# Kernel optimization log

Hardware: AMD Instinct MI355X
Metric: run time of the kernel (lower is better)

## Reference

```python
import jax, jax.numpy as jnp
import numpy as np

B, N, DIM = 8, 4096, 512
H, DH = 8, 64
INNER = H * DH
MIN_FREQ = 1.0 / 64
SCALE = 1.0
ROT_DIM = DH // 2  # 32, per spatial axis
EPS = 1e-5


def setup_inputs() -> dict:
    key = jax.random.key(0)
    ks = jax.random.split(key, 6)
    x = jax.random.normal(ks[0], (B, N, DIM), dtype=jnp.float32)
    pos = jax.random.uniform(ks[1], (B, N, 2), dtype=jnp.float32)
    W_qkv = jax.random.normal(ks[2], (3 * INNER, DIM), dtype=jnp.float32) * (1.0 / DH)
    gamma_k = jnp.ones((DH,), jnp.float32)
    beta_k = jnp.zeros((DH,), jnp.float32)
    gamma_v = jnp.ones((DH,), jnp.float32)
    beta_v = jnp.zeros((DH,), jnp.float32)
    W_out = jax.random.normal(ks[3], (DIM, INNER), dtype=jnp.float32) * (1.0 / np.sqrt(INNER))
    b_out = jnp.zeros((DIM,), jnp.float32)
    return {"x": x, "pos": pos, "W_qkv": W_qkv, "gamma_k": gamma_k, "beta_k": beta_k,
            "gamma_v": gamma_v, "beta_v": beta_v, "W_out": W_out, "b_out": b_out}


def _layernorm(t, gamma, beta):
    mu = jnp.mean(t, axis=-1, keepdims=True)
    var = jnp.var(t, axis=-1, keepdims=True)
    return (t - mu) * jax.lax.rsqrt(var + EPS) * gamma + beta


def _rotate_half(t):
    # '... (j d) -> ... j d' with j=2, then cat(-x2, x1)
    d = t.shape[-1] // 2
    x1, x2 = t[..., :d], t[..., d:]
    return jnp.concatenate((-x2, x1), axis=-1)


def _apply_rot(t, freqs):
    return t * jnp.cos(freqs) + _rotate_half(t) * jnp.sin(freqs)


def _freqs(coord):
    # coord: [b, n]; inv_freq over rotary half-dim
    inv_freq = 1.0 / (10000.0 ** (jnp.arange(0, ROT_DIM, 2, dtype=jnp.float32) / ROT_DIM))
    t = coord * (SCALE / MIN_FREQ)
    f = t[..., None] * inv_freq  # [b, n, ROT_DIM//2]
    return jnp.concatenate((f, f), axis=-1)[:, None, :, :]  # [b, 1, n, ROT_DIM]


def reference(x, pos, W_qkv, gamma_k, beta_k, gamma_v, beta_v, W_out, b_out):
    b, n, _ = x.shape
    qkv = x @ W_qkv.T  # [b, n, 3*INNER]
    q, k, v = jnp.split(qkv, 3, axis=-1)
    split = lambda t: t.reshape(b, n, H, DH).transpose(0, 2, 1, 3)  # b h n d
    q, k, v = split(q), split(k), split(v)

    # Galerkin: LayerNorm on K and V over head dim
    k = _layernorm(k, gamma_k, beta_k)
    v = _layernorm(v, gamma_v, beta_v)

    # 2D rotary on q, k: first half of head dim uses x-coords, second half y-coords
    fx, fy = _freqs(pos[..., 0]), _freqs(pos[..., 1])
    rot2d = lambda t: jnp.concatenate(
        (_apply_rot(t[..., :ROT_DIM], fx), _apply_rot(t[..., ROT_DIM:], fy)), axis=-1)
    q = rot2d(q)
    k = rot2d(k)

    # Associative linear attention: (K^T V) then Q @ (.) / n
    dots = jnp.einsum('bhnd,bhne->bhde', k, v)  # [b, h, d, d]
    out = jnp.einsum('bhnd,bhde->bhne', q, dots) * (1.0 / n)
    out = out.transpose(0, 2, 1, 3).reshape(b, n, INNER)
    return out @ W_out.T + b_out
```

## Files before the change

### kernel.cpp

```cpp
#include <hip/hip_runtime.h>
#include <math.h>

#define NB 8
#define NN 4096
#define NDIM 512
#define NH 8
#define NDH 64
#define QKVC 1536
#define NROWS (NB * NN)
#define EPSF 1e-5f
#define INV_N (1.0f / 4096.0f)
#define L2_10K_16 0.8304820237218406f

typedef __bf16 bf16x8_t __attribute__((ext_vector_type(8)));
typedef float f32x4_t __attribute__((ext_vector_type(4)));
typedef unsigned short u16x8 __attribute__((ext_vector_type(8)));

__device__ inline unsigned short f2bf(float f) {
    unsigned u = __builtin_bit_cast(unsigned, f);
    u += 0x7fff + ((u >> 16) & 1);
    return (unsigned short)(u >> 16);
}
__device__ inline float bf2f(unsigned short u) {
    unsigned v = (unsigned)u << 16;
    return __builtin_bit_cast(float, v);
}

#define GLOAD_LDS16(g, s) __builtin_amdgcn_global_load_lds(                    \
    (const __attribute__((address_space(1))) void*)(g),                        \
    (__attribute__((address_space(3))) void*)(s), 16, 0, 0)

__global__ __launch_bounds__(256)
void cvt_bf16_kernel(const float* __restrict__ s, unsigned short* __restrict__ d, int n)
{
    const int i = (blockIdx.x * 256 + threadIdx.x) * 8;
    if (i >= n) return;
    float4 a = *(const float4*)(s + i);
    float4 b = *(const float4*)(s + i + 4);
    ushort4 lo, hi;
    lo.x = f2bf(a.x); lo.y = f2bf(a.y); lo.z = f2bf(a.z); lo.w = f2bf(a.w);
    hi.x = f2bf(b.x); hi.y = f2bf(b.y); hi.z = f2bf(b.z); hi.w = f2bf(b.w);
    *(ushort4*)(d + i)     = lo;
    *(ushort4*)(d + i + 4) = hi;
}

__global__ __launch_bounds__(256)
void cvt_dots_kernel(const float* __restrict__ s, unsigned short* __restrict__ d)
{
    const int i = (blockIdx.x * 256 + threadIdx.x) * 4;
    float4 a = *(const float4*)(s + i);
    ushort4 o;
    o.x = f2bf(a.x * INV_N); o.y = f2bf(a.y * INV_N);
    o.z = f2bf(a.z * INV_N); o.w = f2bf(a.w * INV_N);
    *(ushort4*)(d + i) = o;
}

__global__ __launch_bounds__(512, 2)
void gemm_qkv_fused(const unsigned short* __restrict__ A,
                    const unsigned short* __restrict__ Bm,
                    const float* __restrict__ pos,
                    const float* __restrict__ gk, const float* __restrict__ bk,
                    const float* __restrict__ gv, const float* __restrict__ bvv,
                    unsigned short* __restrict__ qb,
                    unsigned short* __restrict__ kT,
                    unsigned short* __restrict__ vT)
{
    __shared__ __align__(16) unsigned short lds[2 * 32768];

    const int tid  = threadIdx.x;
    const int wave = tid >> 6;
    const int lane = tid & 63;

    int flat = blockIdx.y * 6 + blockIdx.x;
    flat = (flat & 7) * 96 + (flat >> 3);
    const int bx = flat % 6;
    const int by = flat / 6;
    const int m0 = by * 256;
    const int n0 = bx * 256;

    const int warp_m = wave >> 2;
    const int warp_n = wave & 3;
    const int fr = lane & 15;
    const int fq = lane >> 4;
    const int ch0 = ((fq ^ (fr & 7)) << 3);
    const int ch1 = ch0 ^ 32;

    const int r6 = tid >> 3;
    const int cs = (((tid & 7) ^ (r6 & 7)) << 3);
    const unsigned short* Asrc = A  + (size_t)(m0 + r6) * NDIM + cs;
    const unsigned short* Bsrc = Bm + (size_t)(n0 + (r6 >> 5) * 64 + (r6 & 31)) * NDIM + cs;
    const int sdst = wave * 512;

#define STG_A(tt, h, c) GLOAD_LDS16(Asrc + (size_t)((c) * 128 + (h) * 64) * NDIM + (tt) * 64, \
        &lds[(((tt) & 1) << 15) + ((h) << 13) + ((c) << 12) + sdst])
#define STG_B(tt, h, c) GLOAD_LDS16(Bsrc + (size_t)((c) * 128 + (h) * 32) * NDIM + (tt) * 64, \
        &lds[(((tt) & 1) << 15) + 16384 + ((h) << 13) + ((c) << 12) + sdst])
#define VMCNT4 asm volatile("s_waitcnt vmcnt(4)" ::: "memory")
#define BARF   { __builtin_amdgcn_s_barrier(); asm volatile("" ::: "memory"); }

    f32x4_t acc[8][4] = {};

    STG_A(0, 0, 0); STG_A(0, 0, 1);
    STG_B(0, 0, 0); STG_B(0, 0, 1);
    STG_B(0, 1, 0); STG_B(0, 1, 1);
    STG_A(0, 1, 0); STG_A(0, 1, 1);

    const unsigned short* Afr = &lds[(warp_m * 64 + fr) * 64];
    const unsigned short* Bfr = &lds[16384 + (warp_n * 32 + fr) * 64];

    bf16x8_t a0[4][2], a1[4][2], b0[2][2], b1[2][2];

    for (int tt = 0; tt < 7; ++tt) {
        const int rb = (tt & 1) << 15;
        VMCNT4; BARF;
        #pragma unroll
        for (int mi = 0; mi < 4; ++mi) {
            a0[mi][0] = *(const bf16x8_t*)&Afr[rb + mi * 1024 + ch0];
            a0[mi][1] = *(const bf16x8_t*)&Afr[rb + mi * 1024 + ch1];
        }
        #pragma unroll
        for (int nj = 0; nj < 2; ++nj) {
            b0[nj][0] = *(const bf16x8_t*)&Bfr[rb + nj * 1024 + ch0];
            b0[nj][1] = *(const bf16x8_t*)&Bfr[rb + nj * 1024 + ch1];
        }
        STG_A(tt + 1, 0, 0); STG_A(tt + 1, 0, 1);
        __builtin_amdgcn_s_setprio(1);
        #pragma unroll
        for (int mi = 0; mi < 4; ++mi)
            #pragma unroll
            for (int nj = 0; nj < 2; ++nj) {
                acc[mi][nj] = __builtin_amdgcn_mfma_f32_16x16x32_bf16(a0[mi][0], b0[nj][0], acc[mi][nj], 0, 0, 0);
                acc[mi][nj] = __builtin_amdgcn_mfma_f32_16x16x32_bf16(a0[mi][1], b0[nj][1], acc[mi][nj], 0, 0, 0);
            }
        __builtin_amdgcn_s_setprio(0);
        VMCNT4; BARF;
        #pragma unroll
        for (int nj = 0; nj < 2; ++nj) {
            b1[nj][0] = *(const bf16x8_t*)&Bfr[rb + 8192 + nj * 1024 + ch0];
            b1[nj][1] = *(const bf16x8_t*)&Bfr[rb + 8192 + nj * 1024 + ch1];
        }
        STG_B(tt + 1, 0, 0); STG_B(tt + 1, 0, 1);
        __builtin_amdgcn_s_setprio(1);
        #pragma unroll
        for (int mi = 0; mi < 4; ++mi)
            #pragma unroll
            for (int nj = 0; nj < 2; ++nj) {
                acc[mi][2 + nj] = __builtin_amdgcn_mfma_f32_16x16x32_bf16(a0[mi][0], b1[nj][0], acc[mi][2 + nj], 0, 0, 0);
                acc[mi][2 + nj] = __builtin_amdgcn_mfma_f32_16x16x32_bf16(a0[mi][1], b1[nj][1], acc[mi][2 + nj], 0, 0, 0);
            }
        __builtin_amdgcn_s_setprio(0);
        VMCNT4; BARF;
        #pragma unroll
        for (int mi = 0; mi < 4; ++mi) {
            a1[mi][0] = *(const bf16x8_t*)&Afr[rb + 8192 + mi * 1024 + ch0];
            a1[mi][1] = *(const bf16x8_t*)&Afr[rb + 8192 + mi * 1024 + ch1];
        }
        STG_B(tt + 1, 1, 0); STG_B(tt + 1, 1, 1);
        __builtin_amdgcn_s_setprio(1);
        #pragma unroll
        for (int mi = 0; mi < 4; ++mi)
            #pragma unroll
            for (int nj = 0; nj < 2; ++nj) {
                acc[4 + mi][nj] = __builtin_amdgcn_mfma_f32_16x16x32_bf16(a1[mi][0], b0[nj][0], acc[4 + mi][nj], 0, 0, 0);
                acc[4 + mi][nj] = __builtin_amdgcn_mfma_f32_16x16x32_bf16(a1[mi][1], b0[nj][1], acc[4 + mi][nj], 0, 0, 0);
            }
        __builtin_amdgcn_s_setprio(0);
        STG_A(tt + 1, 1, 0); STG_A(tt + 1, 1, 1);
        __builtin_amdgcn_s_setprio(1);
        #pragma unroll
        for (int mi = 0; mi < 4; ++mi)
            #pragma unroll
            for (int nj = 0; nj < 2; ++nj) {
                acc[4 + mi][2 + nj] = __builtin_amdgcn_mfma_f32_16x16x32_bf16(a1[mi][0], b1[nj][0], acc[4 + mi][2 + nj], 0, 0, 0);
                acc[4 + mi][2 + nj] = __builtin_amdgcn_mfma_f32_16x16x32_bf16(a1[mi][1], b1[nj][1], acc[4 + mi][2 + nj], 0, 0, 0);
            }
        __builtin_amdgcn_s_setprio(0);
    }
    {
        const int rb = 32768;
        asm volatile("s_waitcnt vmcnt(0)" ::: "memory");
        BARF;
        #pragma unroll
        for (int mi = 0; mi < 4; ++mi) {
            a0[mi][0] = *(const bf16x8_t*)&Afr[rb + mi * 1024 + ch0];
            a0[mi][1] = *(const bf16x8_t*)&Afr[rb + mi * 1024 + ch1];
        }
        #pragma unroll
        for (int nj = 0; nj < 2; ++nj) {
            b0[nj][0] = *(const bf16x8_t*)&Bfr[rb + nj * 1024 + ch0];
            b0[nj][1] = *(const bf16x8_t*)&Bfr[rb + nj * 1024 + ch1];
        }
        #pragma unroll
        for (int mi = 0; mi < 4; ++mi)
            #pragma unroll
            for (int nj = 0; nj < 2; ++nj) {
                acc[mi][nj] = __builtin_amdgcn_mfma_f32_16x16x32_bf16(a0[mi][0], b0[nj][0], acc[mi][nj], 0, 0, 0);
                acc[mi][nj] = __builtin_amdgcn_mfma_f32_16x16x32_bf16(a0[mi][1], b0[nj][1], acc[mi][nj], 0, 0, 0);
            }
        #pragma unroll
        for (int nj = 0; nj < 2; ++nj) {
            b1[nj][0] = *(const bf16x8_t*)&Bfr[rb + 8192 + nj * 1024 + ch0];
            b1[nj][1] = *(const bf16x8_t*)&Bfr[rb + 8192 + nj * 1024 + ch1];
        }
        #pragma unroll
        for (int mi = 0; mi < 4; ++mi)
            #pragma unroll
            for (int nj = 0; nj < 2; ++nj) {
                acc[mi][2 + nj] = __builtin_amdgcn_mfma_f32_16x16x32_bf16(a0[mi][0], b1[nj][0], acc[mi][2 + nj], 0, 0, 0);
                acc[mi][2 + nj] = __builtin_amdgcn_mfma_f32_16x16x32_bf16(a0[mi][1], b1[nj][1], acc[mi][2 + nj], 0, 0, 0);
            }
        #pragma unroll
        for (int mi = 0; mi < 4; ++mi) {
            a1[mi][0] = *(const bf16x8_t*)&Afr[rb + 8192 + mi * 1024 + ch0];
            a1[mi][1] = *(const bf16x8_t*)&Afr[rb + 8192 + mi * 1024 + ch1];
        }
        #pragma unroll
        for (int mi = 0; mi < 4; ++mi)
            #pragma unroll
            for (int nj = 0; nj < 2; ++nj) {
                acc[4 + mi][nj] = __builtin_amdgcn_mfma_f32_16x16x32_bf16(a1[mi][0], b0[nj][0], acc[4 + mi][nj], 0, 0, 0);
                acc[4 + mi][nj] = __builtin_amdgcn_mfma_f32_16x16x32_bf16(a1[mi][1], b0[nj][1], acc[4 + mi][nj], 0, 0, 0);
                acc[4 + mi][2 + nj] = __builtin_amdgcn_mfma_f32_16x16x32_bf16(a1[mi][0], b1[nj][0], acc[4 + mi][2 + nj], 0, 0, 0);
                acc[4 + mi][2 + nj] = __builtin_amdgcn_mfma_f32_16x16x32_bf16(a1[mi][1], b1[nj][1], acc[4 + mi][2 + nj], 0, 0, 0);
            }
    }
#undef STG_A
#undef STG_B
#undef VMCNT4
#undef BARF

    const int nc = n0 + warp_n * 64;
    const int type = nc >> 9;
    const int c  = lane & 15;
    const int g4 = (lane >> 4) * 4;
    const int mrow0 = m0 + warp_m * 128;

    if (type != 0) {
        const float* gamma = (type == 1) ? gk : gv;
        const float* beta  = (type == 1) ? bk : bvv;
        float gm[4], bt[4];
        #pragma unroll
        for (int j = 0; j < 4; ++j) { gm[j] = gamma[j * 16 + c]; bt[j] = beta[j * 16 + c]; }
        #pragma unroll
        for (int i = 0; i < 8; ++i)
            #pragma unroll
            for (int r = 0; r < 4; ++r) {
                float t0 = acc[i][0][r], t1 = acc[i][1][r];
                float t2 = acc[i][2][r], t3 = acc[i][3][r];
                float s  = t0 + t1 + t2 + t3;
                float ss = t0*t0 + t1*t1 + t2*t2 + t3*t3;
                #pragma unroll
                for (int msk = 1; msk < 16; msk <<= 1) {
                    s  += __shfl_xor(s,  msk, 64);
                    ss += __shfl_xor(ss, msk, 64);
                }
                const float mu = s * (1.0f / 64.0f);
                const float rs = rsqrtf(ss * (1.0f / 64.0f) - mu * mu + EPSF);
                acc[i][0][r] = (t0 - mu) * rs * gm[0] + bt[0];
                acc[i][1][r] = (t1 - mu) * rs * gm[1] + bt[1];
                acc[i][2][r] = (t2 - mu) * rs * gm[2] + bt[2];
                acc[i][3][r] = (t3 - mu) * rs * gm[3] + bt[3];
            }
    }
    if (type != 2) {
        const float Kc = 64.0f * exp2f(-(float)c * L2_10K_16);
        #pragma unroll
        for (int i = 0; i < 8; ++i)
            #pragma unroll
            for (int r = 0; r < 4; ++r) {
                const int row = mrow0 + (i >> 2) * 64 + (i & 3) * 16 + g4 + r;
                const float2 p = ((const float2*)pos)[row];
                float sx, cx, sy, cy;
                __sincosf(p.x * Kc, &sx, &cx);
                __sincosf(p.y * Kc, &sy, &cy);
                const float t0 = acc[i][0][r], t1 = acc[i][1][r];
                const float t2 = acc[i][2][r], t3 = acc[i][3][r];
                acc[i][0][r] = t0 * cx - t1 * sx;
                acc[i][1][r] = t1 * cx + t0 * sx;
                acc[i][2][r] = t2 * cy - t3 * sy;
                acc[i][3][r] = t3 * cy + t2 * sy;
            }
    }
    if (type == 0) {
        #pragma unroll
        for (int i = 0; i < 8; ++i)
            #pragma unroll
            for (int j = 0; j < 4; ++j) {
                unsigned short* qp = qb
                    + (size_t)(mrow0 + (i >> 2) * 64 + (i & 3) * 16 + g4) * NDIM
                    + nc + j * 16 + c;
                #pragma unroll
                for (int r = 0; r < 4; ++r)
                    qp[(size_t)r * NDIM] = f2bf(acc[i][j][r]);
            }
    } else {
        unsigned short* T = (type == 1) ? kT : vT;
        const int h = (nc >> 6) & 7;
        #pragma unroll
        for (int i = 0; i < 8; ++i) {
            const int row = mrow0 + (i >> 2) * 64 + (i & 3) * 16 + g4;
            const int bb = row >> 12;
            const int nl = row & 4095;
            #pragma unroll
            for (int j = 0; j < 4; ++j) {
                ushort4 o;
                o.x = f2bf(acc[i][j][0]); o.y = f2bf(acc[i][j][1]);
                o.z = f2bf(acc[i][j][2]); o.w = f2bf(acc[i][j][3]);
                *(ushort4*)(T + ((size_t)((bb * NH + h) * 64 + j * 16 + c)) * NN + nl) = o;
            }
        }
    }
}

__global__ __launch_bounds__(256)
void dots_mfma(const unsigned short* __restrict__ kT,
               const unsigned short* __restrict__ vT,
               float* __restrict__ dots)
{
    __shared__ __align__(16) unsigned short sk[2][64 * 64];
    __shared__ __align__(16) unsigned short sv[2][64 * 64];
    const int t = threadIdx.x;
    const int w = t >> 6, l = t & 63;
    const int bh = blockIdx.z * NH + blockIdx.y;
    const int n0 = blockIdx.x * 512;

    const int r8 = l >> 3;
    const int cs = ((l & 7) ^ r8) * 8;
    const unsigned short* ksrc = kT + (size_t)(bh * 64 + w * 16 + r8) * NN + n0 + cs;
    const unsigned short* vsrc = vT + (size_t)(bh * 64 + w * 16 + r8) * NN + n0 + cs;

#define STGK(buf, kt, q) GLOAD_LDS16(ksrc + (size_t)(q) * 8 * NN + (kt), \
        &sk[buf][w * 1024 + (q) * 512])
#define STGV(buf, kt, q) GLOAD_LDS16(vsrc + (size_t)(q) * 8 * NN + (kt), \
        &sv[buf][w * 1024 + (q) * 512])

    const int fr = l & 15, fq = l >> 4;
    const int doff = (w >> 1) * 32, eoff = (w & 1) * 32;

    f32x4_t acc[2][2] = {};

    STGK(0, 0, 0); STGK(0, 0, 1); STGV(0, 0, 0); STGV(0, 0, 1);

    for (int s = 0; s < 8; ++s) {
        const int buf = s & 1;
        asm volatile("s_waitcnt vmcnt(0)" ::: "memory");
        __builtin_amdgcn_s_barrier();
        bf16x8_t ak[2][2], bv[2][2];
        #pragma unroll
        for (int di = 0; di < 2; ++di)
            #pragma unroll
            for (int ks = 0; ks < 2; ++ks)
                ak[di][ks] = *(const bf16x8_t*)
                    &sk[buf][(doff + di * 16 + fr) * 64 + (((ks * 4 + fq) ^ (fr & 7)) * 8)];
        #pragma unroll
        for (int ej = 0; ej < 2; ++ej)
            #pragma unroll
            for (int ks = 0; ks < 2; ++ks)
                bv[ej][ks] = *(const bf16x8_t*)
                    &sv[buf][(eoff + ej * 16 + fr) * 64 + (((ks * 4 + fq) ^ (fr & 7)) * 8)];
        if (s + 1 < 8) {
            const int nb = buf ^ 1, kt = (s + 1) * 64;
            STGK(nb, kt, 0); STGK(nb, kt, 1); STGV(nb, kt, 0); STGV(nb, kt, 1);
        }
        #pragma unroll
        for (int ks = 0; ks < 2; ++ks)
            #pragma unroll
            for (int di = 0; di < 2; ++di)
                #pragma unroll
                for (int ej = 0; ej < 2; ++ej)
                    acc[di][ej] = __builtin_amdgcn_mfma_f32_16x16x32_bf16(
                        ak[di][ks], bv[ej][ks], acc[di][ej], 0, 0, 0);
    }
#undef STGK
#undef STGV

    float* dp = dots + (size_t)bh * 64 * 64;
    const int cc = l & 15;
    const int rr = (l >> 4) * 4;
    #pragma unroll
    for (int di = 0; di < 2; ++di)
        #pragma unroll
        for (int ej = 0; ej < 2; ++ej)
            #pragma unroll
            for (int r = 0; r < 4; ++r)
                atomicAdd(dp + (doff + di * 16 + rr + r) * 64 + eoff + ej * 16 + cc,
                          acc[di][ej][r]);
}

__global__ __launch_bounds__(256)
void dotsw_mfma(const unsigned short* __restrict__ Woutb,
                const unsigned short* __restrict__ dots_bf,
                unsigned short* __restrict__ M2b)
{
    __shared__ unsigned short As[128 * 64];
    __shared__ unsigned short Bs[64 * 64];
    const int t = threadIdx.x;
    const int wave = t >> 6;
    const int lane = t & 63;
    const int dp0 = blockIdx.x * 128;
    const int h = blockIdx.y, b = blockIdx.z;

    const int srow = lane >> 3;
    const int scol = (lane & 7) * 8;
    const unsigned short* Ag = Woutb + (size_t)(dp0 + wave * 32 + srow) * NDIM
                             + h * NDH + scol;
    const unsigned short* Bg = dots_bf + ((size_t)(b * NH + h) * 64 + wave * 16 + srow) * 64
                             + scol;
    #pragma unroll
    for (int i = 0; i < 4; ++i)
        GLOAD_LDS16(Ag + (size_t)i * 8 * NDIM, As + wave * 2048 + i * 512);
    #pragma unroll
    for (int i = 0; i < 2; ++i)
        GLOAD_LDS16(Bg + (size_t)i * 8 * 64, Bs + wave * 1024 + i * 512);
    __syncthreads();

    const int wm = (wave >> 1) * 64;
    const int wn = (wave & 1) * 32;
    const int fr = lane & 15;
    const int fq = (lane >> 4) * 8;

    f32x4_t acc[4][2] = {};
    #pragma unroll
    for (int kk = 0; kk < 2; ++kk) {
        bf16x8_t af[4], bf[2];
        #pragma unroll
        for (int i = 0; i < 4; ++i)
            af[i] = *(const bf16x8_t*)&As[(wm + i * 16 + fr) * 64 + kk * 32 + fq];
        #pragma unroll
        for (int j = 0; j < 2; ++j)
            bf[j] = *(const bf16x8_t*)&Bs[(wn + j * 16 + fr) * 64 + kk * 32 + fq];
        #pragma unroll
        for (int i = 0; i < 4; ++i)
            #pragma unroll
            for (int j = 0; j < 2; ++j)
                acc[i][j] = __builtin_amdgcn_mfma_f32_16x16x32_bf16(
                    af[i], bf[j], acc[i][j], 0, 0, 0);
    }

    const int c  = lane & 15;
    const int g4 = (lane >> 4) * 4;
    #pragma unroll
    for (int i = 0; i < 4; ++i)
        #pragma unroll
        for (int j = 0; j < 2; ++j) {
            unsigned short* mp = M2b + ((size_t)(b * NDIM) + dp0 + wm + i * 16 + g4) * NDIM
                               + h * NDH + wn + j * 16 + c;
            #pragma unroll
            for (int r = 0; r < 4; ++r)
                mp[(size_t)r * NDIM] = f2bf(acc[i][j][r]);
        }
}

__global__ __launch_bounds__(256)
void gemm_out_mfma(const unsigned short* __restrict__ qb,
                   const unsigned short* __restrict__ M2b,
                   const float* __restrict__ bias, float* __restrict__ C)
{
    __shared__ unsigned short As[128 * 32];
    __shared__ unsigned short Bs[128 * 32];
    const int t    = threadIdx.x;
    const int wave = t >> 6;
    const int lane = t & 63;
    const int b  = blockIdx.z;
    const int m0 = b * NN + blockIdx.y * 128;
    const int n0 = blockIdx.x * 128;
    const int wm = (wave >> 1) * 64;
    const int wn = (wave & 1) * 64;
    const int K = NDIM;

    f32x4_t acc[4][4] = {};

    const int srow = wave * 32 + (lane >> 2);
    const int scol = (lane & 3) * 8;
    const unsigned short* Ag = qb + (size_t)(m0 + srow) * NDIM + scol;
    const unsigned short* Bg = M2b + ((size_t)b * NDIM + n0 + srow) * NDIM + scol;
    unsigned short* sA = As + wave * 1024;
    unsigned short* sB = Bs + wave * 1024;

    const int fr = lane & 15;
    const int fq = (lane >> 4) * 8;

    for (int kt = 0; kt < K; kt += 32) {
        __syncthreads();
        GLOAD_LDS16(Ag + kt,             sA);
        GLOAD_LDS16(Ag + kt + 16 * NDIM, sA + 512);
        GLOAD_LDS16(Bg + kt,             sB);
        GLOAD_LDS16(Bg + kt + 16 * NDIM, sB + 512);
        __syncthreads();

        bf16x8_t af[4], bf[4];
        #pragma unroll
        for (int i = 0; i < 4; ++i) {
            af[i] = *(const bf16x8_t*)&As[(wm + i * 16 + fr) * 32 + fq];
            bf[i] = *(const bf16x8_t*)&Bs[(wn + i * 16 + fr) * 32 + fq];
        }
        #pragma unroll
        for (int i = 0; i < 4; ++i)
            #pragma unroll
            for (int j = 0; j < 4; ++j)
                acc[i][j] = __builtin_amdgcn_mfma_f32_16x16x32_bf16(
                    af[i], bf[j], acc[i][j], 0, 0, 0);
    }

    const int crow = (lane >> 4) * 4;
    const int ccol = lane & 15;
    #pragma unroll
    for (int j = 0; j < 4; ++j) {
        const int cn = n0 + wn + j * 16 + ccol;
        const float bb = bias[cn];
        #pragma unroll
        for (int i = 0; i < 4; ++i) {
            float* cp = C + (size_t)(m0 + wm + i * 16 + crow) * NDIM + cn;
            #pragma unroll
            for (int r = 0; r < 4; ++r)
                cp[(size_t)r * NDIM] = acc[i][j][r] + bb;
        }
    }
}

extern "C" void kernel_launch(void* const* d_in, const int* in_sizes, int n_in,
                              void* d_out, int out_size, void* d_ws, size_t ws_size,
                              hipStream_t stream)
{
    const float* x    = (const float*)d_in[0];
    const float* pos  = (const float*)d_in[1];
    const float* Wqkv = (const float*)d_in[2];
    const float* gk   = (const float*)d_in[3];
    const float* bk   = (const float*)d_in[4];
    const float* gv   = (const float*)d_in[5];
    const float* bv   = (const float*)d_in[6];
    const float* Wout = (const float*)d_in[7];
    const float* bout = (const float*)d_in[8];
    float* out = (float*)d_out;

    float* dots = (float*)d_ws;
    unsigned short* dots_bf = (unsigned short*)(dots + (size_t)NB * NH * 64 * 64);
    unsigned short* M2b     = dots_bf + (size_t)NB * NH * 64 * 64;
    unsigned short* qb      = M2b + (size_t)NB * NDIM * NDIM;
    unsigned short* kT      = qb + (size_t)NROWS * NDIM;
    unsigned short* vT      = kT + (size_t)NB * NH * NDH * NN;
    unsigned short* xb      = vT + (size_t)NB * NH * NDH * NN;
    unsigned short* Wqkvb   = xb + (size_t)NROWS * NDIM;
    unsigned short* Woutb   = Wqkvb + (size_t)QKVC * NDIM;

    hipMemsetAsync(dots, 0, (size_t)NB * NH * 64 * 64 * sizeof(float), stream);

    dim3 blk(256);
    cvt_bf16_kernel<<<dim3(NROWS * NDIM / 2048), blk, 0, stream>>>(x, xb, NROWS * NDIM);
    cvt_bf16_kernel<<<dim3(QKVC * NDIM / 2048), blk, 0, stream>>>(Wqkv, Wqkvb, QKVC * NDIM);
    cvt_bf16_kernel<<<dim3(NDIM * NDIM / 2048), blk, 0, stream>>>(Wout, Woutb, NDIM * NDIM);
    gemm_qkv_fused<<<dim3(QKVC / 256, NROWS / 256), dim3(512), 0, stream>>>(
        xb, Wqkvb, pos, gk, bk, gv, bv, qb, kT, vT);
    dots_mfma<<<dim3(NN / 512, NH, NB), blk, 0, stream>>>(kT, vT, dots);
    cvt_dots_kernel<<<dim3(NB * NH * 64 * 64 / 1024), blk, 0, stream>>>(dots, dots_bf);
    dotsw_mfma<<<dim3(NDIM / 128, NH, NB), blk, 0, stream>>>(Woutb, dots_bf, M2b);
    gemm_out_mfma<<<dim3(NDIM / 128, NN / 128, NB), blk, 0, stream>>>(
        qb, M2b, bout, out);
}
```

Before: 285.7 us.

## Fuse conversion kernels, fold dots cast into dotsw, pipeline 256x256 output GEMM

Three separate bf16 conversion launches and the memset of the dots buffer are merged into one cvt_all kernel. The dots-to-bf16 conversion and the 1/n scaling move into dotsw_mfma's shared-memory staging, which removes one launch and one intermediate buffer. The output GEMM is replaced with a 512-thread, 256x256-tile, double-buffered kernel that uses swizzled LDS, async global-to-LDS loads, setprio and grid remapping for cache locality. This cuts launch overhead and raises MFMA utilisation, at the cost of more registers per thread and more complex synchronisation.

```diff
diff --git a/kernel.cpp b/kernel.cpp
--- a/kernel.cpp
+++ b/kernel.cpp
@@ -30,11 +30,9 @@
     (const __attribute__((address_space(1))) void*)(g),                        \
     (__attribute__((address_space(3))) void*)(s), 16, 0, 0)
 
-__global__ __launch_bounds__(256)
-void cvt_bf16_kernel(const float* __restrict__ s, unsigned short* __restrict__ d, int n)
+__device__ inline void cvt8v(const float* __restrict__ s,
+                             unsigned short* __restrict__ d, int i)
 {
-    const int i = (blockIdx.x * 256 + threadIdx.x) * 8;
-    if (i >= n) return;
     float4 a = *(const float4*)(s + i);
     float4 b = *(const float4*)(s + i + 4);
     ushort4 lo, hi;
@@ -45,14 +43,23 @@
 }
 
 __global__ __launch_bounds__(256)
-void cvt_dots_kernel(const float* __restrict__ s, unsigned short* __restrict__ d)
+void cvt_all(const float* __restrict__ x,  const float* __restrict__ wq,
+             const float* __restrict__ wo,
+             unsigned short* __restrict__ xb, unsigned short* __restrict__ wqb,
+             unsigned short* __restrict__ wob, float* __restrict__ dots)
 {
-    const int i = (blockIdx.x * 256 + threadIdx.x) * 4;
-    float4 a = *(const float4*)(s + i);
-    ushort4 o;
-    o.x = f2bf(a.x * INV_N); o.y = f2bf(a.y * INV_N);
-    o.z = f2bf(a.z * INV_N); o.w = f2bf(a.w * INV_N);
-    *(ushort4*)(d + i) = o;
+    const int bid = blockIdx.x, t = threadIdx.x;
+    if (bid < 8192) {
+        cvt8v(x, xb, (bid * 256 + t) * 8);
+    } else if (bid < 8576) {
+        cvt8v(wq, wqb, ((bid - 8192) * 256 + t) * 8);
+    } else if (bid < 8704) {
+        cvt8v(wo, wob, ((bid - 8576) * 256 + t) * 8);
+    } else {
+        const float4 z = {0.f, 0.f, 0.f, 0.f};
+        float4* dp = (float4*)dots + (size_t)((bid - 8704) * 256 + t) * 4;
+        dp[0] = z; dp[1] = z; dp[2] = z; dp[3] = z;
+    }
 }
 
 __global__ __launch_bounds__(512, 2)
@@ -389,7 +396,7 @@
 
 __global__ __launch_bounds__(256)
 void dotsw_mfma(const unsigned short* __restrict__ Woutb,
-                const unsigned short* __restrict__ dots_bf,
+                const float* __restrict__ dots,
                 unsigned short* __restrict__ M2b)
 {
     __shared__ unsigned short As[128 * 64];
@@ -404,14 +411,33 @@
     const int scol = (lane & 7) * 8;
     const unsigned short* Ag = Woutb + (size_t)(dp0 + wave * 32 + srow) * NDIM
                              + h * NDH + scol;
-    const unsigned short* Bg = dots_bf + ((size_t)(b * NH + h) * 64 + wave * 16 + srow) * 64
-                             + scol;
     #pragma unroll
     for (int i = 0; i < 4; ++i)
         GLOAD_LDS16(Ag + (size_t)i * 8 * NDIM, As + wave * 2048 + i * 512);
-    #pragma unroll
-    for (int i = 0; i < 2; ++i)
-        GLOAD_LDS16(Bg + (size_t)i * 8 * 64, Bs + wave * 1024 + i * 512);
+
+    {
+        const float* Dg = dots + (size_t)(b * NH + h) * 4096;
+        const int dr = t >> 2;
+        const int dc = (t & 3) * 16;
+        const float* dgp = Dg + dr * 64 + dc;
+        float4 f0 = *(const float4*)(dgp);
+        float4 f1 = *(const float4*)(dgp + 4);
+        float4 f2 = *(const float4*)(dgp + 8);
+        float4 f3 = *(const float4*)(dgp + 12);
+        ushort4 o0, o1, o2, o3;
+        o0.x = f2bf(f0.x * INV_N); o0.y = f2bf(f0.y * INV_N);
+        o0.z = f2bf(f0.z * INV_N); o0.w = f2bf(f0.w * INV_N);
+        o1.x = f2bf(f1.x * INV_N); o1.y = f2bf(f1.y * INV_N);
+        o1.z = f2bf(f1.z * INV_N); o1.w = f2bf(f1.w * INV_N);
+        o2.x = f2bf(f2.x * INV_N); o2.y = f2bf(f2.y * INV_N);
+        o2.z = f2bf(f2.z * INV_N); o2.w = f2bf(f2.w * INV_N);
+        o3.x = f2bf(f3.x * INV_N); o3.y = f2bf(f3.y * INV_N);
+        o3.z = f2bf(f3.z * INV_N); o3.w = f2bf(f3.w * INV_N);
+        *(ushort4*)&Bs[dr * 64 + dc]      = o0;
+        *(ushort4*)&Bs[dr * 64 + dc + 4]  = o1;
+        *(ushort4*)&Bs[dr * 64 + dc + 8]  = o2;
+        *(ushort4*)&Bs[dr * 64 + dc + 12] = o3;
+    }
     __syncthreads();
 
     const int wm = (wave >> 1) * 64;
@@ -451,66 +477,190 @@
         }
 }
 
-__global__ __launch_bounds__(256)
-void gemm_out_mfma(const unsigned short* __restrict__ qb,
-                   const unsigned short* __restrict__ M2b,
-                   const float* __restrict__ bias, float* __restrict__ C)
+__global__ __launch_bounds__(512, 2)
+void gemm_out_mfma256(const unsigned short* __restrict__ qb,
+                      const unsigned short* __restrict__ M2b,
+                      const float* __restrict__ bias, float* __restrict__ C)
 {
-    __shared__ unsigned short As[128 * 32];
-    __shared__ unsigned short Bs[128 * 32];
-    const int t    = threadIdx.x;
-    const int wave = t >> 6;
-    const int lane = t & 63;
-    const int b  = blockIdx.z;
-    const int m0 = b * NN + blockIdx.y * 128;
-    const int n0 = blockIdx.x * 128;
-    const int wm = (wave >> 1) * 64;
-    const int wn = (wave & 1) * 64;
-    const int K = NDIM;
-
-    f32x4_t acc[4][4] = {};
-
-    const int srow = wave * 32 + (lane >> 2);
-    const int scol = (lane & 3) * 8;
-    const unsigned short* Ag = qb + (size_t)(m0 + srow) * NDIM + scol;
-    const unsigned short* Bg = M2b + ((size_t)b * NDIM + n0 + srow) * NDIM + scol;
-    unsigned short* sA = As + wave * 1024;
-    unsigned short* sB = Bs + wave * 1024;
-
+    __shared__ __align__(16) unsigned short lds[2 * 32768];
+
+    const int tid  = threadIdx.x;
+    const int wave = tid >> 6;
+    const int lane = tid & 63;
+
+    int flat = blockIdx.y * 2 + blockIdx.x;
+    flat = (flat & 7) * 32 + (flat >> 3);
+    const int bx = flat & 1;
+    const int by = flat >> 1;
+    const int m0 = by * 256;
+    const int n0 = bx * 256;
+    const int b  = m0 >> 12;
+
+    const int warp_m = wave >> 2;
+    const int warp_n = wave & 3;
     const int fr = lane & 15;
-    const int fq = (lane >> 4) * 8;
-
-    for (int kt = 0; kt < K; kt += 32) {
-        __syncthreads();
-        GLOAD_LDS16(Ag + kt,             sA);
-        GLOAD_LDS16(Ag + kt + 16 * NDIM, sA + 512);
-        GLOAD_LDS16(Bg + kt,             sB);
-        GLOAD_LDS16(Bg + kt + 16 * NDIM, sB + 512);
-        __syncthreads();
-
-        bf16x8_t af[4], bf[4];
-        #pragma unroll
-        for (int i = 0; i < 4; ++i) {
-            af[i] = *(const bf16x8_t*)&As[(wm + i * 16 + fr) * 32 + fq];
-            bf[i] = *(const bf16x8_t*)&Bs[(wn + i * 16 + fr) * 32 + fq];
-        }
-        #pragma unroll
-        for (int i = 0; i < 4; ++i)
-            #pragma unroll
-            for (int j = 0; j < 4; ++j)
-                acc[i][j] = __builtin_amdgcn_mfma_f32_16x16x32_bf16(
-                    af[i], bf[j], acc[i][j], 0, 0, 0);
-    }
-
-    const int crow = (lane >> 4) * 4;
-    const int ccol = lane & 15;
+    const int fq = lane >> 4;
+    const int ch0 = ((fq ^ (fr & 7)) << 3);
+    const int ch1 = ch0 ^ 32;
+
+    const int r6 = tid >> 3;
+    const int cs = (((tid & 7) ^ (r6 & 7)) << 3);
+    const unsigned short* Asrc = qb + (size_t)(m0 + r6) * NDIM + cs;
+    const unsigned short* Bsrc = M2b + (size_t)b * NDIM * NDIM
+                               + (size_t)(n0 + (r6 >> 5) * 64 + (r6 & 31)) * NDIM + cs;
+    const int sdst = wave * 512;
+
+#define STG_A(tt, h, c) GLOAD_LDS16(Asrc + (size_t)((c) * 128 + (h) * 64) * NDIM + (tt) * 64, \
+        &lds[(((tt) & 1) << 15) + ((h) << 13) + ((c) << 12) + sdst])
+#define STG_B(tt, h, c) GLOAD_LDS16(Bsrc + (size_t)((c) * 128 + (h) * 32) * NDIM + (tt) * 64, \
+        &lds[(((tt) & 1) << 15) + 16384 + ((h) << 13) + ((c) << 12) + sdst])
+#define VMCNT4 asm volatile("s_waitcnt vmcnt(4)" ::: "memory")
+#define BARF   { __builtin_amdgcn_s_barrier(); asm volatile("" ::: "memory"); }
+
+    f32x4_t acc[8][4] = {};
+
+    STG_A(0, 0, 0); STG_A(0, 0, 1);
+    STG_B(0, 0, 0); STG_B(0, 0, 1);
+    STG_B(0, 1, 0); STG_B(0, 1, 1);
+    STG_A(0, 1, 0); STG_A(0, 1, 1);
+
+    const unsigned short* Afr = &lds[(warp_m * 64 + fr) * 64];
+    const unsigned short* Bfr = &lds[16384 + (warp_n * 32 + fr) * 64];
+
+    bf16x8_t a0[4][2], a1[4][2], b0[2][2], b1[2][2];
+
+    for (int tt = 0; tt < 7; ++tt) {
+        const int rb = (tt & 1) << 15;
+        VMCNT4; BARF;
+        #pragma unroll
+        for (int mi = 0; mi < 4; ++mi) {
+            a0[mi][0] = *(const bf16x8_t*)&Afr[rb + mi * 1024 + ch0];
+            a0[mi][1] = *(const bf16x8_t*)&Afr[rb + mi * 1024 + ch1];
+        }
+        #pragma unroll
+        for (int nj = 0; nj < 2; ++nj) {
+            b0[nj][0] = *(const bf16x8_t*)&Bfr[rb + nj * 1024 + ch0];
+            b0[nj][1] = *(const bf16x8_t*)&Bfr[rb + nj * 1024 + ch1];
+        }
+        STG_A(tt + 1, 0, 0); STG_A(tt + 1, 0, 1);
+        __builtin_amdgcn_s_setprio(1);
+        #pragma unroll
+        for (int mi = 0; mi < 4; ++mi)
+            #pragma unroll
+            for (int nj = 0; nj < 2; ++nj) {
+                acc[mi][nj] = __builtin_amdgcn_mfma_f32_16x16x32_bf16(a0[mi][0], b0[nj][0], acc[mi][nj], 0, 0, 0);
+                acc[mi][nj] = __builtin_amdgcn_mfma_f32_16x16x32_bf16(a0[mi][1], b0[nj][1], acc[mi][nj], 0, 0, 0);
+            }
+        __builtin_amdgcn_s_setprio(0);
+        VMCNT4; BARF;
+        #pragma unroll
+        for (int nj = 0; nj < 2; ++nj) {
+            b1[nj][0] = *(const bf16x8_t*)&Bfr[rb + 8192 + nj * 1024 + ch0];
+            b1[nj][1] = *(const bf16x8_t*)&Bfr[rb + 8192 + nj * 1024 + ch1];
+        }
+        STG_B(tt + 1, 0, 0); STG_B(tt + 1, 0, 1);
+        __builtin_amdgcn_s_setprio(1);
+        #pragma unroll
+        for (int mi = 0; mi < 4; ++mi)
+            #pragma unroll
+            for (int nj = 0; nj < 2; ++nj) {
+                acc[mi][2 + nj] = __builtin_amdgcn_mfma_f32_16x16x32_bf16(a0[mi][0], b1[nj][0], acc[mi][2 + nj], 0, 0, 0);
+                acc[mi][2 + nj] = __builtin_amdgcn_mfma_f32_16x16x32_bf16(a0[mi][1], b1[nj][1], acc[mi][2 + nj], 0, 0, 0);
+            }
+        __builtin_amdgcn_s_setprio(0);
+        VMCNT4; BARF;
+        #pragma unroll
+        for (int mi = 0; mi < 4; ++mi) {
+            a1[mi][0] = *(const bf16x8_t*)&Afr[rb + 8192 + mi * 1024 + ch0];
+            a1[mi][1] = *(const bf16x8_t*)&Afr[rb + 8192 + mi * 1024 + ch1];
+        }
+        STG_B(tt + 1, 1, 0); STG_B(tt + 1, 1, 1);
+        __builtin_amdgcn_s_setprio(1);
+        #pragma unroll
+        for (int mi = 0; mi < 4; ++mi)
+            #pragma unroll
+            for (int nj = 0; nj < 2; ++nj) {
+                acc[4 + mi][nj] = __builtin_amdgcn_mfma_f32_16x16x32_bf16(a1[mi][0], b0[nj][0], acc[4 + mi][nj], 0, 0, 0);
+                acc[4 + mi][nj] = __builtin_amdgcn_mfma_f32_16x16x32_bf16(a1[mi][1], b0[nj][1], acc[4 + mi][nj], 0, 0, 0);
+            }
+        __builtin_amdgcn_s_setprio(0);
+        STG_A(tt + 1, 1, 0); STG_A(tt + 1, 1, 1);
+        __builtin_amdgcn_s_setprio(1);
+        #pragma unroll
+        for (int mi = 0; mi < 4; ++mi)
+            #pragma unroll
+            for (int nj = 0; nj < 2; ++nj) {
+                acc[4 + mi][2 + nj] = __builtin_amdgcn_mfma_f32_16x16x32_bf16(a1[mi][0], b1[nj][0], acc[4 + mi][2 + nj], 0, 0, 0);
+                acc[4 + mi][2 + nj] = __builtin_amdgcn_mfma_f32_16x16x32_bf16(a1[mi][1], b1[nj][1], acc[4 + mi][2 + nj], 0, 0, 0);
+            }
+        __builtin_amdgcn_s_setprio(0);
+    }
+    {
+        const int rb = 32768;
+        asm volatile("s_waitcnt vmcnt(0)" ::: "memory");
+        BARF;
+        #pragma unroll
+        for (int mi = 0; mi < 4; ++mi) {
+            a0[mi][0] = *(const bf16x8_t*)&Afr[rb + mi * 1024 + ch0];
+            a0[mi][1] = *(const bf16x8_t*)&Afr[rb + mi * 1024 + ch1];
+        }
+        #pragma unroll
+        for (int nj = 0; nj < 2; ++nj) {
+            b0[nj][0] = *(const bf16x8_t*)&Bfr[rb + nj * 1024 + ch0];
+            b0[nj][1] = *(const bf16x8_t*)&Bfr[rb + nj * 1024 + ch1];
+        }
+        #pragma unroll
+        for (int mi = 0; mi < 4; ++mi)
+            #pragma unroll
+            for (int nj = 0; nj < 2; ++nj) {
+                acc[mi][nj] = __builtin_amdgcn_mfma_f32_16x16x32_bf16(a0[mi][0], b0[nj][0], acc[mi][nj], 0, 0, 0);
+                acc[mi][nj] = __builtin_amdgcn_mfma_f32_16x16x32_bf16(a0[mi][1], b0[nj][1], acc[mi][nj], 0, 0, 0);
+            }
+        #pragma unroll
+        for (int nj = 0; nj < 2; ++nj) {
+            b1[nj][0] = *(const bf16x8_t*)&Bfr[rb + 8192 + nj * 1024 + ch0];
+            b1[nj][1] = *(const bf16x8_t*)&Bfr[rb + 8192 + nj * 1024 + ch1];
+        }
+        #pragma unroll
+        for (int mi = 0; mi < 4; ++mi)
+            #pragma unroll
+            for (int nj = 0; nj < 2; ++nj) {
+                acc[mi][2 + nj] = __builtin_amdgcn_mfma_f32_16x16x32_bf16(a0[mi][0], b1[nj][0], acc[mi][2 + nj], 0, 0, 0);
+                acc[mi][2 + nj] = __builtin_amdgcn_mfma_f32_16x16x32_bf16(a0[mi][1], b1[nj][1], acc[mi][2 + nj], 0, 0, 0);
+            }
+        #pragma unroll
+        for (int mi = 0; mi < 4; ++mi) {
+            a1[mi][0] = *(const bf16x8_t*)&Afr[rb + 8192 + mi * 1024 + ch0];
+            a1[mi][1] = *(const bf16x8_t*)&Afr[rb + 8192 + mi * 1024 + ch1];
+        }
+        #pragma unroll
+        for (int mi = 0; mi < 4; ++mi)
+            #pragma unroll
+            for (int nj = 0; nj < 2; ++nj) {
+                acc[4 + mi][nj] = __builtin_amdgcn_mfma_f32_16x16x32_bf16(a1[mi][0], b0[nj][0], acc[4 + mi][nj], 0, 0, 0);
+                acc[4 + mi][nj] = __builtin_amdgcn_mfma_f32_16x16x32_bf16(a1[mi][1], b0[nj][1], acc[4 + mi][nj], 0, 0, 0);
+                acc[4 + mi][2 + nj] = __builtin_amdgcn_mfma_f32_16x16x32_bf16(a1[mi][0], b1[nj][0], acc[4 + mi][2 + nj], 0, 0, 0);
+                acc[4 + mi][2 + nj] = __builtin_amdgcn_mfma_f32_16x16x32_bf16(a1[mi][1], b1[nj][1], acc[4 + mi][2 + nj], 0, 0, 0);
+            }
+    }
+#undef STG_A
+#undef STG_B
+#undef VMCNT4
+#undef BARF
+
+    const int c  = lane & 15;
+    const int g4 = (lane >> 4) * 4;
+    const int mrow0 = m0 + warp_m * 128;
+    const int ncol = n0 + warp_n * 64;
+
     #pragma unroll
     for (int j = 0; j < 4; ++j) {
-        const int cn = n0 + wn + j * 16 + ccol;
-        const float bb = bias[cn];
-        #pragma unroll
-        for (int i = 0; i < 4; ++i) {
-            float* cp = C + (size_t)(m0 + wm + i * 16 + crow) * NDIM + cn;
+        const int col = ncol + j * 16 + c;
+        const float bb = bias[col];
+        #pragma unroll
+        for (int i = 0; i < 8; ++i) {
+            const int row = mrow0 + (i >> 2) * 64 + (i & 3) * 16 + g4;
+            float* cp = C + (size_t)row * NDIM + col;
             #pragma unroll
             for (int r = 0; r < 4; ++r)
                 cp[(size_t)r * NDIM] = acc[i][j][r] + bb;
@@ -534,8 +684,7 @@
     float* out = (float*)d_out;
 
     float* dots = (float*)d_ws;
-    unsigned short* dots_bf = (unsigned short*)(dots + (size_t)NB * NH * 64 * 64);
-    unsigned short* M2b     = dots_bf + (size_t)NB * NH * 64 * 64;
+    unsigned short* M2b     = (unsigned short*)(dots + (size_t)NB * NH * 64 * 64);
     unsigned short* qb      = M2b + (size_t)NB * NDIM * NDIM;
     unsigned short* kT      = qb + (size_t)NROWS * NDIM;
     unsigned short* vT      = kT + (size_t)NB * NH * NDH * NN;
@@ -543,17 +692,11 @@
     unsigned short* Wqkvb   = xb + (size_t)NROWS * NDIM;
     unsigned short* Woutb   = Wqkvb + (size_t)QKVC * NDIM;
 
-    hipMemsetAsync(dots, 0, (size_t)NB * NH * 64 * 64 * sizeof(float), stream);
-
-    dim3 blk(256);
-    cvt_bf16_kernel<<<dim3(NROWS * NDIM / 2048), blk, 0, stream>>>(x, xb, NROWS * NDIM);
-    cvt_bf16_kernel<<<dim3(QKVC * NDIM / 2048), blk, 0, stream>>>(Wqkv, Wqkvb, QKVC * NDIM);
-    cvt_bf16_kernel<<<dim3(NDIM * NDIM / 2048), blk, 0, stream>>>(Wout, Woutb, NDIM * NDIM);
+    cvt_all<<<dim3(8768), dim3(256), 0, stream>>>(x, Wqkv, Wout, xb, Wqkvb, Woutb, dots);
     gemm_qkv_fused<<<dim3(QKVC / 256, NROWS / 256), dim3(512), 0, stream>>>(
         xb, Wqkvb, pos, gk, bk, gv, bv, qb, kT, vT);
-    dots_mfma<<<dim3(NN / 512, NH, NB), blk, 0, stream>>>(kT, vT, dots);
-    cvt_dots_kernel<<<dim3(NB * NH * 64 * 64 / 1024), blk, 0, stream>>>(dots, dots_bf);
-    dotsw_mfma<<<dim3(NDIM / 128, NH, NB), blk, 0, stream>>>(Woutb, dots_bf, M2b);
-    gemm_out_mfma<<<dim3(NDIM / 128, NN / 128, NB), blk, 0, stream>>>(
+    dots_mfma<<<dim3(NN / 512, NH, NB), dim3(256), 0, stream>>>(kT, vT, dots);
+    dotsw_mfma<<<dim3(NDIM / 128, NH, NB), dim3(256), 0, stream>>>(Woutb, dots, M2b);
+    gemm_out_mfma256<<<dim3(2, NROWS / 256), dim3(512), 0, stream>>>(
         qb, M2b, bout, out);
 }
```

Result: faster. 278.0 us (-2.7%).
